# Performance work log

Hardware: AMD Instinct MI355X
Metric: run time of the kernel (lower is better)

## Reference

```python
import jax, jax.numpy as jnp
import numpy as np

NEG_SLOPE = 0.2

def _l2norm(x):
    # F.normalize(x, 2, -1): x / max(||x||_2, 1e-12)
    return x / jnp.maximum(jnp.linalg.norm(x, axis=-1, keepdims=True), 1e-12)

def _segment_softmax(e, dst, n_dst):
    m = jax.ops.segment_max(e, dst, num_segments=n_dst)
    m = jnp.where(jnp.isfinite(m), m, 0.0)
    ex = jnp.exp(e - m[dst])
    denom = jax.ops.segment_sum(ex, dst, num_segments=n_dst)
    return ex / (denom[dst] + 1e-16)

def _gat_conv(x_src, x_dst, edge_index, W, a_src, a_dst, b, n_dst):
    # PyG GATConv, heads=1, concat, shared lin for src/dst (int in_channels)
    h_src = x_src @ W                      # [Ns, H]
    h_dst = x_dst @ W                      # [Nd, H]
    src, dst = edge_index[0], edge_index[1]
    al_s = h_src @ a_src                   # [Ns]
    al_d = h_dst @ a_dst                   # [Nd]
    e = jax.nn.leaky_relu(al_s[src] + al_d[dst], NEG_SLOPE)  # [E]
    coef = _segment_softmax(e, dst, n_dst)                   # [E]
    out = jax.ops.segment_sum(coef[:, None] * h_src[src], dst, num_segments=n_dst)
    return out + b

def setup_inputs() -> dict:
    key = jax.random.key(0)
    ks = jax.random.split(key, 32)
    nd, npr, nc, H, L, B = 2000, 19000, 100, 256, 2, 8192
    E_pp, E_dp, E_cp = 400000, 60000, 300000
    s = 0.1
    inp = {
        'drug_emb': jax.random.normal(ks[0], (nd, H), jnp.float32),
        'protein_emb': jax.random.normal(ks[1], (npr, H), jnp.float32),
        'cell_emb': jax.random.normal(ks[2], (nc, H), jnp.float32),
        'W_pp': jax.random.normal(ks[3], (L, H, H), jnp.float32) * s,
        'as_pp': jax.random.normal(ks[4], (L, H), jnp.float32) * s,
        'ad_pp': jax.random.normal(ks[5], (L, H), jnp.float32) * s,
        'b_pp': jax.random.normal(ks[6], (L, H), jnp.float32) * s,
        'W_dp': jax.random.normal(ks[7], (L, H, H), jnp.float32) * s,
        'as_dp': jax.random.normal(ks[8], (L, H), jnp.float32) * s,
        'ad_dp': jax.random.normal(ks[9], (L, H), jnp.float32) * s,
        'b_dp': jax.random.normal(ks[10], (L, H), jnp.float32) * s,
        'W_cp': jax.random.normal(ks[11], (L, H, H), jnp.float32) * s,
        'as_cp': jax.random.normal(ks[12], (L, H), jnp.float32) * s,
        'ad_cp': jax.random.normal(ks[13], (L, H), jnp.float32) * s,
        'b_cp': jax.random.normal(ks[14], (L, H), jnp.float32) * s,
        'W1': jax.random.normal(ks[15], (3 * H, 6 * H), jnp.float32) * s,
        'b1': jax.random.normal(ks[16], (6 * H,), jnp.float32) * s,
        'W2': jax.random.normal(ks[17], (6 * H, 2 * H), jnp.float32) * s,
        'b2': jax.random.normal(ks[18], (2 * H,), jnp.float32) * s,
        'W3': jax.random.normal(ks[19], (2 * H, 2), jnp.float32) * s,
        'b3': jax.random.normal(ks[20], (2,), jnp.float32) * s,
        'edge_pp': jnp.stack([jax.random.randint(ks[21], (E_pp,), 0, npr),
                              jax.random.randint(ks[22], (E_pp,), 0, npr)]),
        'edge_dp': jnp.stack([jax.random.randint(ks[23], (E_dp,), 0, npr),
                              jax.random.randint(ks[24], (E_dp,), 0, nd)]),
        'edge_cp': jnp.stack([jax.random.randint(ks[25], (E_cp,), 0, npr),
                              jax.random.randint(ks[26], (E_cp,), 0, nc)]),
        'drug1': jax.random.randint(ks[27], (B,), 0, nd),
        'drug2': jax.random.randint(ks[28], (B,), 0, nd),
        'cell': jax.random.randint(ks[29], (B,), 0, nc),
    }
    return inp

def reference(drug_emb, protein_emb, cell_emb,
              W_pp, as_pp, ad_pp, b_pp,
              W_dp, as_dp, ad_dp, b_dp,
              W_cp, as_cp, ad_cp, b_cp,
              W1, b1, W2, b2, W3, b3,
              edge_pp, edge_dp, edge_cp, drug1, drug2, cell):
    n_drug, n_prot, n_cell = drug_emb.shape[0], protein_emb.shape[0], cell_emb.shape[0]
    num_layer = W_pp.shape[0]
    # node ids are arange -> embedding lookup is the full table
    x_d, x_p, x_c = drug_emb, protein_emb, cell_emb
    # p-p GATConv adds self loops (default add_self_loops=True)
    loop = jnp.arange(n_prot, dtype=edge_pp.dtype)
    ei_pp = jnp.concatenate([edge_pp, jnp.stack([loop, loop])], axis=1)
    for l in range(num_layer):
        x_p = _gat_conv(x_p, x_p, ei_pp, W_pp[l], as_pp[l], ad_pp[l], b_pp[l], n_prot)
        x_p = _l2norm(x_p)
        x_d = jax.nn.relu(_gat_conv(x_p, x_d, edge_dp, W_dp[l], as_dp[l], ad_dp[l], b_dp[l], n_drug))
        x_c = jax.nn.relu(_gat_conv(x_p, x_c, edge_cp, W_cp[l], as_cp[l], ad_cp[l], b_cp[l], n_cell))
    hid = jnp.concatenate([_l2norm(x_d[drug1]), _l2norm(x_d[drug2]), _l2norm(x_c[cell])], axis=1)
    h = jax.nn.relu(hid @ W1 + b1)
    h = jax.nn.relu(h @ W2 + b2)
    logits = h @ W3 + b3
    return logits
```

## Files before the change

### kernel.cpp

```cpp
#include <hip/hip_runtime.h>
#include <hip/hip_bf16.h>

#define HDIM 256
#define NEG_SLOPE 0.2f
#define NB 128
#define SLICES 8
#define TBN 64
#define TBK 32

typedef __attribute__((ext_vector_type(8))) short bf16x8;
typedef __attribute__((ext_vector_type(4))) float f32x4;

__device__ inline uint f2pl(float x) {
  __hip_bfloat16 h = __float2bfloat16(x);
  ushort hi = *(ushort*)&h;
  float r = x - __bfloat162float(h);
  __hip_bfloat16 l = __float2bfloat16(r);
  ushort lo = *(ushort*)&l;
  return (uint)hi | ((uint)lo << 16);
}
__device__ inline ushort f2b(float x) {
  __hip_bfloat16 h = __float2bfloat16(x);
  return *(ushort*)&h;
}
__device__ inline float b2f(ushort u) {
  uint x = ((uint)u) << 16;
  return __int_as_float((int)x);
}

static inline int cdiv(int a, int b) { return (a + b - 1) / b; }

__global__ void fillf_kernel(float* __restrict__ p, float v, int n) {
  int i = blockIdx.x * blockDim.x + threadIdx.x;
  if (i < n) p[i] = v;
}

__global__ void fill_out2_kernel(float* __restrict__ out, const float* __restrict__ b3, int M) {
  int i = blockIdx.x * 256 + threadIdx.x;
  if (i >= M) return;
  out[(size_t)i * 2 + 0] = b3[0];
  out[(size_t)i * 2 + 1] = b3[1];
}

__global__ void wconv_split_kernel(const float* __restrict__ W,
                                   ushort* __restrict__ WTh, ushort* __restrict__ WTl,
                                   int K, int N) {
  int i = blockIdx.x * 256 + threadIdx.x;
  if (i >= K * N) return;
  int k = i / N, n = i - k * N;
  uint p = f2pl(W[i]);
  WTh[(size_t)n * K + k] = (ushort)(p & 0xffff);
  WTl[(size_t)n * K + k] = (ushort)(p >> 16);
}

__global__ void wconv_split3_kernel(
    const float* __restrict__ Wpp, const float* __restrict__ Wdp, const float* __restrict__ Wcp,
    ushort* __restrict__ WTpph, ushort* __restrict__ WTppl,
    ushort* __restrict__ WTdph, ushort* __restrict__ WTdpl,
    ushort* __restrict__ WTcph, ushort* __restrict__ WTcpl, int L) {
  const int per = HDIM * HDIM;
  int i = blockIdx.x * 256 + threadIdx.x;
  if (i >= 3 * L * per) return;
  int mat = i / per;
  int r = i - mat * per;
  int l = mat / 3, ty = mat - l * 3;
  const float* W = (ty == 0 ? Wpp : ty == 1 ? Wdp : Wcp) + (size_t)l * per;
  ushort* Th = (ty == 0 ? WTpph : ty == 1 ? WTdph : WTcph) + (size_t)l * per;
  ushort* Tl = (ty == 0 ? WTppl : ty == 1 ? WTdpl : WTcpl) + (size_t)l * per;
  int k = r >> 8, n = r & (HDIM - 1);
  uint p = f2pl(W[r]);
  Th[(size_t)n * HDIM + k] = (ushort)(p & 0xffff);
  Tl[(size_t)n * HDIM + k] = (ushort)(p >> 16);
}

__global__ void f32_to_b16_kernel(const float* __restrict__ in, ushort* __restrict__ out, int n) {
  int i = blockIdx.x * 256 + threadIdx.x;
  if (i < n) out[i] = f2b(in[i]);
}

__global__ void f32_to_split_kernel(const float* __restrict__ in,
                                    ushort* __restrict__ oh, ushort* __restrict__ ol, int n) {
  int i = blockIdx.x * 256 + threadIdx.x;
  if (i >= n) return;
  uint p = f2pl(in[i]);
  oh[i] = (ushort)(p & 0xffff);
  ol[i] = (ushort)(p >> 16);
}

__global__ __launch_bounds__(256) void matvec_all_kernel(
    const float* __restrict__ Wpp, const float* __restrict__ aspp, const float* __restrict__ adpp,
    const float* __restrict__ Wdp, const float* __restrict__ asdp, const float* __restrict__ addp,
    const float* __restrict__ Wcp, const float* __restrict__ ascp, const float* __restrict__ adcp,
    float* __restrict__ wv) {
  int b = blockIdx.x;
  int l = b / 6, r = b - l * 6, type = r >> 1, isd = r & 1;
  const float* W = (type == 0 ? Wpp : type == 1 ? Wdp : Wcp) + (size_t)l * HDIM * HDIM;
  const float* a = (type == 0 ? (isd ? adpp : aspp)
                  : type == 1 ? (isd ? addp : asdp)
                              : (isd ? adcp : ascp)) + (size_t)l * HDIM;
  int k = threadIdx.x;
  const float4* Wr = (const float4*)(W + (size_t)k * HDIM);
  float s = 0.f;
#pragma unroll 8
  for (int n4 = 0; n4 < HDIM / 4; ++n4) {
    float4 w = Wr[n4];
    float4 av = *(const float4*)(a + n4 * 4);
    s += w.x * av.x + w.y * av.y + w.z * av.z + w.w * av.w;
  }
  wv[(size_t)b * HDIM + k] = s;
}

__global__ __launch_bounds__(256) void combine_h1_kernel(
    const float* __restrict__ P1, const float* __restrict__ P2, const float* __restrict__ P3,
    const int* __restrict__ g1, const int* __restrict__ g2, const int* __restrict__ g3,
    int row0, ushort* __restrict__ h1h, ushort* __restrict__ h1l, int M, int K) {
  int t = blockIdx.x * 256 + threadIdx.x;
  int kq = K >> 2;
  if (t >= M * kq) return;
  int row = t / kq, c4 = t - row * kq;
  int bi = row0 + row;
  size_t o = (size_t)c4 * 4;
  float4 a = *(const float4*)(P1 + (size_t)g1[bi] * K + o);
  float4 b = *(const float4*)(P2 + (size_t)g2[bi] * K + o);
  float4 c = *(const float4*)(P3 + (size_t)g3[bi] * K + o);
  uint p0 = f2pl(fmaxf(a.x + b.x + c.x, 0.f));
  uint p1 = f2pl(fmaxf(a.y + b.y + c.y, 0.f));
  uint p2 = f2pl(fmaxf(a.z + b.z + c.z, 0.f));
  uint p3 = f2pl(fmaxf(a.w + b.w + c.w, 0.f));
  ushort4 h = {(ushort)(p0 & 0xffff), (ushort)(p1 & 0xffff), (ushort)(p2 & 0xffff), (ushort)(p3 & 0xffff)};
  ushort4 l = {(ushort)(p0 >> 16), (ushort)(p1 >> 16), (ushort)(p2 >> 16), (ushort)(p3 >> 16)};
  *(ushort4*)(h1h + (size_t)row * K + o) = h;
  *(ushort4*)(h1l + (size_t)row * K + o) = l;
}

template <int TBM_, int ACT, int FUSE3>
__global__ __launch_bounds__(256) void mfma_gemm(
    const ushort* __restrict__ Ahg, const ushort* __restrict__ Alg,
    const ushort* __restrict__ Bhg, const ushort* __restrict__ Blg,
    int ldb, const float* __restrict__ bias, const float* __restrict__ W3g,
    float* __restrict__ C, int M, int N, int K) {
  __shared__ __align__(16) ushort Ah[2][4][TBM_][8];
  __shared__ __align__(16) ushort Al[2][4][TBM_][8];
  __shared__ __align__(16) ushort Bh[2][4][TBN][8];
  __shared__ __align__(16) ushort Bl[2][4][TBN][8];

  constexpr int NU = TBM_ / 64;
  constexpr int TM = TBM_ / 32;

  const int tid = threadIdx.x;
  const int lane = tid & 63;
  const int wid = tid >> 6;
  const int wm = wid & 1, wn = wid >> 1;
  const int l16 = lane & 15;
  const int quad = lane >> 4;
  const int m0 = blockIdx.x * TBM_;
  const int n0 = blockIdx.y * TBN;

  const int gq = lane & 3;
  const int co = gq * 8;
  const int r4 = lane >> 2;

  uint4 rah0[NU], ral0[NU], rbh0, rbl0;
  uint4 rah1[NU], ral1[NU], rbh1, rbl1;

  auto LOADA = [&](uint4* rah, uint4* ral, uint4& rbh, uint4& rbl, int k0) {
#pragma unroll
    for (int u = 0; u < NU; ++u) {
      int r = wid * (TBM_ / 4) + r4 + 16 * u;
      int gm = m0 + r;
      if (gm < M) {
        size_t o = (size_t)gm * K + k0 + co;
        rah[u] = *(const uint4*)(Ahg + o);
        ral[u] = *(const uint4*)(Alg + o);
      } else {
        rah[u] = make_uint4(0, 0, 0, 0);
        ral[u] = make_uint4(0, 0, 0, 0);
      }
    }
    {
      int r = wid * 16 + r4;
      size_t o = (size_t)(n0 + r) * ldb + k0 + co;
      rbh = *(const uint4*)(Bhg + o);
      rbl = *(const uint4*)(Blg + o);
    }
  };
  auto STORE = [&](const uint4* rah, const uint4* ral, const uint4& rbh, const uint4& rbl, int b) {
#pragma unroll
    for (int u = 0; u < NU; ++u) {
      int r = wid * (TBM_ / 4) + r4 + 16 * u;
      *(uint4*)&Ah[b][gq][r][0] = rah[u];
      *(uint4*)&Al[b][gq][r][0] = ral[u];
    }
    int r = wid * 16 + r4;
    *(uint4*)&Bh[b][gq][r][0] = rbh;
    *(uint4*)&Bl[b][gq][r][0] = rbl;
  };

  f32x4 acc[TM][2];
#pragma unroll
  for (int i = 0; i < TM; ++i)
#pragma unroll
    for (int j = 0; j < 2; ++j) acc[i][j] = (f32x4){0.f, 0.f, 0.f, 0.f};

  auto COMPUTE = [&](int b) {
    bf16x8 ahf[TM], alf[TM], bhf[2], blf[2];
#pragma unroll
    for (int t = 0; t < TM; ++t) {
      int r = wm * (TBM_ / 2) + t * 16 + l16;
      ahf[t] = *(const bf16x8*)&Ah[b][quad][r][0];
      alf[t] = *(const bf16x8*)&Al[b][quad][r][0];
    }
#pragma unroll
    for (int t = 0; t < 2; ++t) {
      int r = wn * 32 + t * 16 + l16;
      bhf[t] = *(const bf16x8*)&Bh[b][quad][r][0];
      blf[t] = *(const bf16x8*)&Bl[b][quad][r][0];
    }
#pragma unroll
    for (int tm = 0; tm < TM; ++tm)
#pragma unroll
      for (int tn = 0; tn < 2; ++tn) {
        acc[tm][tn] = __builtin_amdgcn_mfma_f32_16x16x32_bf16(ahf[tm], bhf[tn], acc[tm][tn], 0, 0, 0);
        acc[tm][tn] = __builtin_amdgcn_mfma_f32_16x16x32_bf16(ahf[tm], blf[tn], acc[tm][tn], 0, 0, 0);
        acc[tm][tn] = __builtin_amdgcn_mfma_f32_16x16x32_bf16(alf[tm], bhf[tn], acc[tm][tn], 0, 0, 0);
      }
  };

  const int NK = K / TBK;
  LOADA(rah0, ral0, rbh0, rbl0, 0);
  LOADA(rah1, ral1, rbh1, rbl1, TBK);
  STORE(rah0, ral0, rbh0, rbl0, 0);
  int k = 2 * TBK;
  for (int t = 0; t < (NK - 2) / 2; ++t) {
    __syncthreads();
    LOADA(rah0, ral0, rbh0, rbl0, k);
    COMPUTE(0);
    STORE(rah1, ral1, rbh1, rbl1, 1);
    k += TBK;
    __syncthreads();
    LOADA(rah1, ral1, rbh1, rbl1, k);
    COMPUTE(1);
    STORE(rah0, ral0, rbh0, rbl0, 0);
    k += TBK;
  }
  __syncthreads();
  COMPUTE(0);
  STORE(rah1, ral1, rbh1, rbl1, 1);
  __syncthreads();
  COMPUTE(1);

  if (FUSE3) {
#pragma unroll
    for (int tm = 0; tm < TM; ++tm) {
#pragma unroll
      for (int r = 0; r < 4; ++r) {
        int row = m0 + wm * (TBM_ / 2) + tm * 16 + quad * 4 + r;
        float s0 = 0.f, s1 = 0.f;
#pragma unroll
        for (int tn = 0; tn < 2; ++tn) {
          int col = n0 + wn * 32 + tn * 16 + l16;
          float v = fmaxf(acc[tm][tn][r] + bias[col], 0.f);
          s0 += v * W3g[col * 2 + 0];
          s1 += v * W3g[col * 2 + 1];
        }
#pragma unroll
        for (int o = 1; o < 16; o <<= 1) {
          s0 += __shfl_xor(s0, o);
          s1 += __shfl_xor(s1, o);
        }
        if (l16 == 0 && row < M) {
          atomicAdd(&C[(size_t)row * 2 + 0], s0);
          atomicAdd(&C[(size_t)row * 2 + 1], s1);
        }
      }
    }
  } else {
#pragma unroll
    for (int tn = 0; tn < 2; ++tn) {
      int col = n0 + wn * 32 + tn * 16 + l16;
      float bv = bias ? bias[col] : 0.f;
#pragma unroll
      for (int tm = 0; tm < TM; ++tm) {
#pragma unroll
        for (int r = 0; r < 4; ++r) {
          int row = m0 + wm * (TBM_ / 2) + tm * 16 + quad * 4 + r;
          if (row >= M) continue;
          float v = acc[tm][tn][r] + bv;
          if (ACT == 1) v = fmaxf(v, 0.f);
          C[(size_t)row * N + col] = v;
        }
      }
    }
  }
}

template <int TBM_, int ACT>
static void gemm_launch(hipStream_t s,
                        const ushort* Ahg, const ushort* Alg,
                        const ushort* Bhg, const ushort* Blg,
                        int ldb, const float* bias, float* C,
                        int M, int N, int K) {
  dim3 g(cdiv(M, TBM_), N / TBN);
  mfma_gemm<TBM_, ACT, 0><<<g, 256, 0, s>>>(Ahg, Alg, Bhg, Blg, ldb, bias, nullptr, C, M, N, K);
}

static void gemm_launch_f3(hipStream_t s,
                           const ushort* Ahg, const ushort* Alg,
                           const ushort* Bhg, const ushort* Blg,
                           int ldb, const float* bias, const float* W3,
                           float* C, int M, int N, int K) {
  dim3 g(cdiv(M, 128), N / TBN);
  mfma_gemm<128, 1, 1><<<g, 256, 0, s>>>(Ahg, Alg, Bhg, Blg, ldb, bias, W3, C, M, N, K);
}

__global__ __launch_bounds__(256) void rowdot_kernel(
    const float* __restrict__ H, const float* __restrict__ a,
    float* __restrict__ out, int n) {
  int row = blockIdx.x * 4 + (threadIdx.x >> 6);
  if (row >= n) return;
  int lane = threadIdx.x & 63;
  const float* h = H + (size_t)row * HDIM;
  float s = 0.f;
#pragma unroll
  for (int u = 0; u < 4; ++u) {
    int c = lane + u * 64;
    s += h[c] * a[c];
  }
#pragma unroll
  for (int off = 32; off; off >>= 1) s += __shfl_down(s, off);
  if (lane == 0) out[row] = s;
}

__global__ __launch_bounds__(256) void rowdot2_kernel(
    const float* __restrict__ H, const float* __restrict__ a1, const float* __restrict__ a2,
    float* __restrict__ o1, float* __restrict__ o2, int n) {
  int row = blockIdx.x * 4 + (threadIdx.x >> 6);
  if (row >= n) return;
  int lane = threadIdx.x & 63;
  const float* h = H + (size_t)row * HDIM;
  float s1 = 0.f, s2 = 0.f;
#pragma unroll
  for (int u = 0; u < 4; ++u) {
    int c = lane + u * 64;
    float hv = h[c];
    s1 += hv * a1[c];
    s2 += hv * a2[c];
  }
#pragma unroll
  for (int off = 32; off; off >>= 1) {
    s1 += __shfl_down(s1, off);
    s2 += __shfl_down(s2, off);
  }
  if (lane == 0) { o1[row] = s1; o2[row] = s2; }
}

__global__ __launch_bounds__(256) void hist_kernel(
    const int* __restrict__ src, const int* __restrict__ dst, int E, int nloops,
    int Nd, int* __restrict__ offs) {
  extern __shared__ int bins[];
  int tot = E + nloops;
  int chunk = (tot + NB - 1) / NB;
  int b = blockIdx.x;
  int s0 = b * chunk, s1 = min(s0 + chunk, tot);
  for (int i = threadIdx.x; i < Nd; i += 256) bins[i] = 0;
  __syncthreads();
  for (int i = s0 + threadIdx.x; i < s1; i += 256) {
    int d = (i < E) ? dst[i] : (i - E);
    atomicAdd(&bins[d], 1);
  }
  __syncthreads();
  for (int i = threadIdx.x; i < Nd; i += 256) offs[(size_t)i * NB + b] = bins[i];
}

__global__ __launch_bounds__(256) void scan_bins_kernel(
    int* __restrict__ offs, int* __restrict__ binsum, int Nd) {
  int d = blockIdx.x * 4 + (threadIdx.x >> 6);
  if (d >= Nd) return;
  int lane = threadIdx.x & 63;
  int* p = offs + (size_t)d * NB;
  int v0 = p[2 * lane], v1 = p[2 * lane + 1];
  int s = v0 + v1;
  int t = s;
#pragma unroll
  for (int o = 1; o < 64; o <<= 1) { int u = __shfl_up(t, o); if (lane >= o) t += u; }
  int excl = t - s;
  p[2 * lane] = excl;
  p[2 * lane + 1] = excl + v0;
  if (lane == 63) binsum[d] = t;
}

__global__ __launch_bounds__(256) void scan_base_kernel(
    const int* __restrict__ binsum, int* __restrict__ rowptr, int Nd) {
  __shared__ int wsum[4];
  __shared__ int carry;
  if (threadIdx.x == 0) carry = 0;
  __syncthreads();
  int lane = threadIdx.x & 63, w = threadIdx.x >> 6;
  for (int t0 = 0; t0 < Nd; t0 += 256) {
    int i = t0 + threadIdx.x;
    int v = (i < Nd) ? binsum[i] : 0;
    int t = v;
#pragma unroll
    for (int o = 1; o < 64; o <<= 1) { int u = __shfl_up(t, o); if (lane >= o) t += u; }
    if (lane == 63) wsum[w] = t;
    __syncthreads();
    int add = carry;
    for (int k = 0; k < w; ++k) add += wsum[k];
    if (i < Nd) rowptr[i] = t - v + add;
    __syncthreads();
    if (threadIdx.x == 0) carry += wsum[0] + wsum[1] + wsum[2] + wsum[3];
    __syncthreads();
  }
  if (threadIdx.x == 0) rowptr[Nd] = carry;
}

__global__ __launch_bounds__(256) void scatter_kernel(
    const int* __restrict__ src, const int* __restrict__ dst, int E, int nloops,
    int Nd, const int* __restrict__ offs, const int* __restrict__ rowptr,
    uint* __restrict__ sd) {
  extern __shared__ int bins[];
  int tot = E + nloops;
  int chunk = (tot + NB - 1) / NB;
  int b = blockIdx.x;
  int s0 = b * chunk, s1 = min(s0 + chunk, tot);
  for (int i = threadIdx.x; i < Nd; i += 256) bins[i] = 0;
  __syncthreads();
  for (int i = s0 + threadIdx.x; i < s1; i += 256) {
    int s_, d_;
    if (i < E) { s_ = src[i]; d_ = dst[i]; }
    else       { s_ = d_ = i - E; }
    int local = atomicAdd(&bins[d_], 1);
    int pos = rowptr[d_] + offs[(size_t)d_ * NB + b] + local;
    sd[pos] = (uint)s_ | ((uint)d_ << 16);
  }
}

__global__ __launch_bounds__(256) void gat_agg_split(
    const int* __restrict__ rowptr, const uint* __restrict__ sd,
    const float* __restrict__ als, const float* __restrict__ ald,
    const ushort* __restrict__ Xb,
    ushort* __restrict__ aggh, ushort* __restrict__ aggl, int n) {
  int d = blockIdx.x * 4 + (threadIdx.x >> 6);
  if (d >= n) return;
  int lane = threadIdx.x & 63;
  int r0 = rowptr[d], r1 = rowptr[d + 1];
  float aldd = ald[d];
  float dsum = 0.f;
  for (int j = r0 + lane; j < r1; j += 64) {
    float e = als[sd[j] & 0xffff] + aldd;
    e = (e > 0.f) ? e : NEG_SLOPE * e;
    dsum += __expf(e);
  }
#pragma unroll
  for (int o = 32; o; o >>= 1) dsum += __shfl_xor(dsum, o);
  float rden = 1.f / (dsum + 1e-16f);

  float4 acc = make_float4(0.f, 0.f, 0.f, 0.f);
  for (int b = r0; b < r1; b += 64) {
    int j = b + lane;
    float exv = 0.f; int srcv = 0;
    if (j < r1) {
      uint p = sd[j];
      srcv = p & 0xffff;
      float e = als[srcv] + aldd;
      e = (e > 0.f) ? e : NEG_SLOPE * e;
      exv = __expf(e) * rden;
    }
    int cnt = min(64, r1 - b);
    for (int t0 = 0; t0 < cnt; t0 += 8) {
      float cf[8]; int sv[8];
#pragma unroll
      for (int u = 0; u < 8; ++u) {
        cf[u] = __shfl(exv, t0 + u);
        sv[u] = __shfl(srcv, t0 + u);
      }
      ushort4 hv[8];
#pragma unroll
      for (int u = 0; u < 8; ++u)
        hv[u] = *(const ushort4*)(Xb + (size_t)sv[u] * HDIM + lane * 4);
#pragma unroll
      for (int u = 0; u < 8; ++u) {
        acc.x += cf[u] * b2f(hv[u].x);
        acc.y += cf[u] * b2f(hv[u].y);
        acc.z += cf[u] * b2f(hv[u].z);
        acc.w += cf[u] * b2f(hv[u].w);
      }
    }
  }
  uint p0 = f2pl(acc.x), p1 = f2pl(acc.y), p2 = f2pl(acc.z), p3 = f2pl(acc.w);
  ushort4 h = {(ushort)(p0 & 0xffff), (ushort)(p1 & 0xffff), (ushort)(p2 & 0xffff), (ushort)(p3 & 0xffff)};
  ushort4 l = {(ushort)(p0 >> 16), (ushort)(p1 >> 16), (ushort)(p2 >> 16), (ushort)(p3 >> 16)};
  *(ushort4*)(aggh + (size_t)d * HDIM + lane * 4) = h;
  *(ushort4*)(aggl + (size_t)d * HDIM + lane * 4) = l;
}

__global__ __launch_bounds__(256) void gat_agg_slice(
    const int* __restrict__ rowptr, const uint* __restrict__ sd,
    const float* __restrict__ als, const float* __restrict__ ald,
    const ushort* __restrict__ Xb, float* __restrict__ out32, int n) {
  int d = blockIdx.x / SLICES;
  int sl = blockIdx.x - d * SLICES;
  if (d >= n) return;
  int lane = threadIdx.x & 63, w = threadIdx.x >> 6;
  int r0 = rowptr[d], r1 = rowptr[d + 1];
  float aldd = ald[d];
  float dsum = 0.f;
  for (int j = r0 + threadIdx.x; j < r1; j += 256) {
    float e = als[sd[j] & 0xffff] + aldd;
    e = (e > 0.f) ? e : NEG_SLOPE * e;
    dsum += __expf(e);
  }
#pragma unroll
  for (int o = 32; o; o >>= 1) dsum += __shfl_xor(dsum, o);
  __shared__ float wd[4];
  if (lane == 0) wd[w] = dsum;
  __syncthreads();
  float rden = 1.f / (wd[0] + wd[1] + wd[2] + wd[3] + 1e-16f);
  int deg = r1 - r0;
  int per_b = (deg + SLICES - 1) / SLICES;
  int b0 = r0 + sl * per_b, b1 = min(b0 + per_b, r1);
  int wdeg = b1 - b0;
  if (wdeg <= 0) return;
  int per_w = (wdeg + 3) >> 2;
  int w0 = b0 + w * per_w, w1 = min(w0 + per_w, b1);

  float4 acc = make_float4(0.f, 0.f, 0.f, 0.f);
  for (int b = w0; b < w1; b += 64) {
    int j = b + lane;
    float exv = 0.f; int srcv = 0;
    if (j < w1) {
      uint p = sd[j];
      srcv = p & 0xffff;
      float e = als[srcv] + aldd;
      e = (e > 0.f) ? e : NEG_SLOPE * e;
      exv = __expf(e) * rden;
    }
    int cnt = min(64, w1 - b);
    for (int t0 = 0; t0 < cnt; t0 += 8) {
      float cf[8]; int sv[8];
#pragma unroll
      for (int u = 0; u < 8; ++u) {
        cf[u] = __shfl(exv, t0 + u);
        sv[u] = __shfl(srcv, t0 + u);
      }
      ushort4 hv[8];
#pragma unroll
      for (int u = 0; u < 8; ++u)
        hv[u] = *(const ushort4*)(Xb + (size_t)sv[u] * HDIM + lane * 4);
#pragma unroll
      for (int u = 0; u < 8; ++u) {
        acc.x += cf[u] * b2f(hv[u].x);
        acc.y += cf[u] * b2f(hv[u].y);
        acc.z += cf[u] * b2f(hv[u].z);
        acc.w += cf[u] * b2f(hv[u].w);
      }
    }
  }
  float* o = out32 + (size_t)d * HDIM + lane * 4;
  atomicAdd(o + 0, acc.x); atomicAdd(o + 1, acc.y);
  atomicAdd(o + 2, acc.z); atomicAdd(o + 3, acc.w);
}

__global__ __launch_bounds__(256) void l2norm_f32b_dots_kernel(
    const float* __restrict__ in, float* __restrict__ outf, ushort* __restrict__ outb,
    const float* __restrict__ v1, const float* __restrict__ v2,
    const float* __restrict__ v3, const float* __restrict__ v4,
    float* __restrict__ o1, float* __restrict__ o2,
    float* __restrict__ o3, float* __restrict__ o4, int n) {
  int row = blockIdx.x * 4 + (threadIdx.x >> 6);
  if (row >= n) return;
  int lane = threadIdx.x & 63;
  float v[4];
  float ss = 0.f;
#pragma unroll
  for (int u = 0; u < 4; ++u) {
    float t = in[(size_t)row * HDIM + lane + u * 64];
    v[u] = t; ss += t * t;
  }
#pragma unroll
  for (int off = 32; off; off >>= 1) ss += __shfl_xor(ss, off);
  float sc = 1.0f / fmaxf(sqrtf(ss), 1e-12f);
  float d1 = 0.f, d2 = 0.f, d3 = 0.f, d4 = 0.f;
#pragma unroll
  for (int u = 0; u < 4; ++u) {
    float f = v[u] * sc;
    int c = lane + u * 64;
    outf[(size_t)row * HDIM + c] = f;
    outb[(size_t)row * HDIM + c] = f2b(f);
    d1 += f * v1[c];
    d2 += f * v2[c];
    if (o3) { d3 += f * v3[c]; d4 += f * v4[c]; }
  }
#pragma unroll
  for (int off = 32; off; off >>= 1) {
    d1 += __shfl_xor(d1, off);
    d2 += __shfl_xor(d2, off);
    if (o3) { d3 += __shfl_xor(d3, off); d4 += __shfl_xor(d4, off); }
  }
  if (lane == 0) {
    o1[row] = d1; o2[row] = d2;
    if (o3) { o3[row] = d3; o4[row] = d4; }
  }
}

__global__ __launch_bounds__(256) void l2norm_split_kernel(
    const float* __restrict__ in,
    ushort* __restrict__ oh, ushort* __restrict__ ol, int n) {
  int row = blockIdx.x * 4 + (threadIdx.x >> 6);
  if (row >= n) return;
  int lane = threadIdx.x & 63;
  float v[4];
  float ss = 0.f;
#pragma unroll
  for (int u = 0; u < 4; ++u) {
    int c = lane + u * 64;
    float t = in[(size_t)row * HDIM + c];
    v[u] = t;
    ss += t * t;
  }
#pragma unroll
  for (int off = 32; off; off >>= 1) ss += __shfl_xor(ss, off);
  float sc = 1.0f / fmaxf(sqrtf(ss), 1e-12f);
#pragma unroll
  for (int u = 0; u < 4; ++u) {
    int c = lane + u * 64;
    uint p = f2pl(v[u] * sc);
    oh[(size_t)row * HDIM + c] = (ushort)(p & 0xffff);
    ol[(size_t)row * HDIM + c] = (ushort)(p >> 16);
  }
}

static void build_sorted(hipStream_t stream,
                         const int* src, const int* dst, int E, int nloops, int Nd,
                         int* offs, int* binsum, int* rowptr, uint* sd) {
  size_t lds = (size_t)Nd * sizeof(int);
  hist_kernel<<<NB, 256, lds, stream>>>(src, dst, E, nloops, Nd, offs);
  scan_bins_kernel<<<cdiv(Nd, 4), 256, 0, stream>>>(offs, binsum, Nd);
  scan_base_kernel<<<1, 256, 0, stream>>>(binsum, rowptr, Nd);
  scatter_kernel<<<NB, 256, lds, stream>>>(src, dst, E, nloops, Nd, offs, rowptr, sd);
}

extern "C" void kernel_launch(void* const* d_in, const int* in_sizes, int n_in,
                              void* d_out, int out_size, void* d_ws, size_t ws_size,
                              hipStream_t stream) {
  const float* drug_emb = (const float*)d_in[0];
  const float* prot_emb = (const float*)d_in[1];
  const float* cell_emb = (const float*)d_in[2];
  const float* W_pp = (const float*)d_in[3];
  const float* as_pp = (const float*)d_in[4];
  const float* ad_pp = (const float*)d_in[5];
  const float* b_pp = (const float*)d_in[6];
  const float* W_dp = (const float*)d_in[7];
  const float* as_dp = (const float*)d_in[8];
  const float* ad_dp = (const float*)d_in[9];
  const float* b_dp = (const float*)d_in[10];
  const float* W_cp = (const float*)d_in[11];
  const float* as_cp = (const float*)d_in[12];
  const float* ad_cp = (const float*)d_in[13];
  const float* b_cp = (const float*)d_in[14];
  const float* W1 = (const float*)d_in[15];
  const float* b1 = (const float*)d_in[16];
  const float* W2 = (const float*)d_in[17];
  const float* b2 = (const float*)d_in[18];
  const float* W3 = (const float*)d_in[19];
  const float* b3 = (const float*)d_in[20];
  const int* edge_pp = (const int*)d_in[21];
  const int* edge_dp = (const int*)d_in[22];
  const int* edge_cp = (const int*)d_in[23];
  const int* drug1 = (const int*)d_in[24];
  const int* drug2 = (const int*)d_in[25];
  const int* cellb = (const int*)d_in[26];

  const int ND = in_sizes[0] / HDIM;
  const int NP = in_sizes[1] / HDIM;
  const int NC = in_sizes[2] / HDIM;
  const int L = in_sizes[3] / (HDIM * HDIM);
  const int E_pp = in_sizes[21] / 2;
  const int E_dp = in_sizes[22] / 2;
  const int E_cp = in_sizes[23] / 2;
  const int B = in_sizes[24];
  (void)n_in; (void)out_size;

  const int* src_pp = edge_pp;          const int* dst_pp = edge_pp + E_pp;
  const int* src_dp = edge_dp;          const int* dst_dp = edge_dp + E_dp;
  const int* src_cp = edge_cp;          const int* dst_cp = edge_cp + E_cp;
  const int tot_pp = E_pp + NP, tot_dp = E_dp, tot_cp = E_cp;
  int maxN = NP > ND ? NP : ND; if (NC > maxN) maxN = NC;

  char* wsb = (char*)d_ws;
  size_t off = 0;
  auto alloc = [&](size_t bytes) -> void* {
    void* p = wsb + off;
    off += (bytes + 255) & ~(size_t)255;
    return p;
  };

  float* Xp  = (float*)alloc((size_t)NP * HDIM * 4);
  ushort* Xpb = (ushort*)alloc((size_t)NP * HDIM * 2);
  float* Xd  = (float*)alloc((size_t)ND * HDIM * 4);
  float* Xc  = (float*)alloc((size_t)NC * HDIM * 4);
  ushort* xdnh = (ushort*)alloc((size_t)ND * HDIM * 2);
  ushort* xdnl = (ushort*)alloc((size_t)ND * HDIM * 2);
  ushort* xcnh = (ushort*)alloc((size_t)NC * HDIM * 2);
  ushort* xcnl = (ushort*)alloc((size_t)NC * HDIM * 2);
  ushort* WTpph = (ushort*)alloc((size_t)L * HDIM * HDIM * 2);
  ushort* WTppl = (ushort*)alloc((size_t)L * HDIM * HDIM * 2);
  ushort* WTdph = (ushort*)alloc((size_t)L * HDIM * HDIM * 2);
  ushort* WTdpl = (ushort*)alloc((size_t)L * HDIM * HDIM * 2);
  ushort* WTcph = (ushort*)alloc((size_t)L * HDIM * HDIM * 2);
  ushort* WTcpl = (ushort*)alloc((size_t)L * HDIM * HDIM * 2);
  ushort* cth = (ushort*)alloc((size_t)NC * HDIM * 2);
  ushort* ctl = (ushort*)alloc((size_t)NC * HDIM * 2);
  float* wv  = (float*)alloc((size_t)L * 6 * HDIM * 4);
  float* pals = (float*)alloc((size_t)maxN * 4);
  float* pald = (float*)alloc((size_t)maxN * 4);
  float* als1 = (float*)alloc((size_t)maxN * 4);
  float* als2 = (float*)alloc((size_t)maxN * 4);
  float* ald1 = (float*)alloc((size_t)maxN * 4);
  float* ald2 = (float*)alloc((size_t)maxN * 4);
  int* binsum = (int*)alloc((size_t)maxN * 4);
  int* rp_pp = (int*)alloc((size_t)(NP + 1) * 4);
  int* rp_dp = (int*)alloc((size_t)(ND + 1) * 4);
  int* rp_cp = (int*)alloc((size_t)(NC + 1) * 4);
  uint* sd_pp = (uint*)alloc((size_t)tot_pp * 4);
  uint* sd_dp = (uint*)alloc((size_t)tot_dp * 4);
  uint* sd_cp = (uint*)alloc((size_t)tot_cp * 4);
  float* out32 = (float*)alloc((size_t)NC * HDIM * 4);
  size_t S0 = off;

  int* offs = (int*)(wsb + S0);
  build_sorted(stream, src_pp, dst_pp, E_pp, NP, NP, offs, binsum, rp_pp, sd_pp);
  build_sorted(stream, src_dp, dst_dp, E_dp, 0, ND, offs, binsum, rp_dp, sd_dp);
  build_sorted(stream, src_cp, dst_cp, E_cp, 0, NC, offs, binsum, rp_cp, sd_cp);

  wconv_split3_kernel<<<cdiv(3 * L * HDIM * HDIM, 256), 256, 0, stream>>>(
      W_pp, W_dp, W_cp, WTpph, WTppl, WTdph, WTdpl, WTcph, WTcpl, L);
  matvec_all_kernel<<<L * 6, 256, 0, stream>>>(W_pp, as_pp, ad_pp, W_dp, as_dp, ad_dp,
                                               W_cp, as_cp, ad_cp, wv);
  f32_to_b16_kernel<<<cdiv(NP * HDIM, 256), 256, 0, stream>>>(prot_emb, Xpb, NP * HDIM);

  size_t aggB = ((size_t)NP * HDIM * 2 + 255) & ~(size_t)255;
  ushort* aggh = (ushort*)(wsb + S0);
  ushort* aggl = (ushort*)(wsb + S0 + aggB);
  float* tmp = (float*)(wsb + S0 + 2 * aggB);

  rowdot2_kernel<<<cdiv(NP, 4), 256, 0, stream>>>(prot_emb, wv + 0 * HDIM, wv + 1 * HDIM,
                                                  pals, pald, NP);

  for (int l = 0; l < L; ++l) {
    const int WOFF = l * HDIM * HDIM, VOFF = l * HDIM;
    const float* wvl = wv + (size_t)l * 6 * HDIM;
    const float* wvn = wv + (size_t)(l + 1) * 6 * HDIM;
    const float* Xd_cur = (l == 0) ? drug_emb : Xd;
    const float* Xc_cur = (l == 0) ? cell_emb : Xc;
    bool last = (l == L - 1);

    gat_agg_split<<<cdiv(NP, 4), 256, 0, stream>>>(rp_pp, sd_pp, pals, pald, Xpb, aggh, aggl, NP);
    gemm_launch<128, 0>(stream, aggh, aggl, WTpph + WOFF, WTppl + WOFF, HDIM,
                        b_pp + VOFF, tmp, NP, HDIM, HDIM);
    l2norm_f32b_dots_kernel<<<cdiv(NP, 4), 256, 0, stream>>>(
        tmp, Xp, Xpb,
        wvl + 2 * HDIM, wvl + 4 * HDIM,
        last ? nullptr : (wvn + 0 * HDIM), last ? nullptr : (wvn + 1 * HDIM),
        als1, als2, last ? nullptr : pals, last ? nullptr : pald, NP);

    rowdot_kernel<<<cdiv(ND, 4), 256, 0, stream>>>(Xd_cur, wvl + 3 * HDIM, ald1, ND);
    rowdot_kernel<<<cdiv(NC, 4), 256, 0, stream>>>(Xc_cur, wvl + 5 * HDIM, ald2, NC);

    gat_agg_split<<<cdiv(ND, 4), 256, 0, stream>>>(rp_dp, sd_dp, als1, ald1, Xpb, aggh, aggl, ND);
    gemm_launch<64, 1>(stream, aggh, aggl, WTdph + WOFF, WTdpl + WOFF, HDIM,
                       b_dp + VOFF, Xd, ND, HDIM, HDIM);

    fillf_kernel<<<cdiv(NC * HDIM, 256), 256, 0, stream>>>(out32, 0.f, NC * HDIM);
    gat_agg_slice<<<NC * SLICES, 256, 0, stream>>>(rp_cp, sd_cp, als2, ald2, Xpb, out32, NC);
    f32_to_split_kernel<<<cdiv(NC * HDIM, 256), 256, 0, stream>>>(out32, cth, ctl, NC * HDIM);
    gemm_launch<64, 1>(stream, cth, ctl, WTcph + WOFF, WTcpl + WOFF, HDIM,
                       b_cp + VOFF, Xc, NC, HDIM, HDIM);
  }

  l2norm_split_kernel<<<cdiv(ND, 4), 256, 0, stream>>>(Xd, xdnh, xdnl, ND);
  l2norm_split_kernel<<<cdiv(NC, 4), 256, 0, stream>>>(Xc, xcnh, xcnl, NC);

  const int N1 = 6 * HDIM;
  const int N2 = 2 * HDIM;
  const int K1 = 3 * HDIM;
  ushort* W1Th = (ushort*)(wsb + S0);
  ushort* W1Tl = W1Th + (size_t)N1 * K1;
  ushort* W2Th = W1Tl + (size_t)N1 * K1;
  ushort* W2Tl = W2Th + (size_t)N2 * N1;
  float* P1 = (float*)(W2Tl + (size_t)N2 * N1);
  float* P2 = P1 + (size_t)ND * N1;
  float* P3 = P2 + (size_t)ND * N1;
  ushort* h1h = (ushort*)(P3 + (size_t)NC * N1);
  size_t wsz = ws_size ? ws_size : ((size_t)1 << 30);
  size_t fixed = S0 + ((size_t)N1 * K1 + (size_t)N2 * N1) * 4
               + ((size_t)(2 * ND + NC) * N1) * 4;
  int CH = 8192;
  while (CH > 1024 && fixed + (size_t)CH * N1 * 4 > wsz) CH >>= 1;
  ushort* h1l = h1h + (size_t)CH * N1;

  wconv_split_kernel<<<cdiv(K1 * N1, 256), 256, 0, stream>>>(W1, W1Th, W1Tl, K1, N1);
  wconv_split_kernel<<<cdiv(N1 * N2, 256), 256, 0, stream>>>(W2, W2Th, W2Tl, N1, N2);

  gemm_launch<64, 0>(stream, xdnh, xdnl, W1Th, W1Tl, K1, nullptr, P1, ND, N1, HDIM);
  gemm_launch<64, 0>(stream, xdnh, xdnl, W1Th + HDIM, W1Tl + HDIM, K1, nullptr, P2, ND, N1, HDIM);
  gemm_launch<64, 0>(stream, xcnh, xcnl, W1Th + 2 * HDIM, W1Tl + 2 * HDIM, K1, b1, P3, NC, N1, HDIM);

  float* outp = (float*)d_out;
  fill_out2_kernel<<<cdiv(B, 256), 256, 0, stream>>>(outp, b3, B);
  for (int c0 = 0; c0 < B; c0 += CH) {
    int M = (B - c0) < CH ? (B - c0) : CH;
    combine_h1_kernel<<<cdiv(M * (N1 / 4), 256), 256, 0, stream>>>(
        P1, P2, P3, drug1, drug2, cellb, c0, h1h, h1l, M, N1);
    gemm_launch_f3(stream, h1h, h1l, W2Th, W2Tl, N1, b2, W3,
                   outp + (size_t)c0 * 2, M, N2, N1);
  }
}
```

Before: 714.9 us.

## Swizzle GEMM LDS layout to avoid bank conflicts and fuse protein prep kernels

Reorganizes the MFMA GEMM shared-memory tiles into 16-row chunks with an XOR-like slot rotation based on the k-quad, so that stores and fragment loads spread across LDS banks instead of conflicting. It also fuses the f32-to-bf16 conversion of the protein embedding with the two attention row-dot products into one kernel, which saves a full extra read of the protein table and one launch. The swizzle adds index arithmetic and must stay consistent between store and load paths. The wvn pointer change only avoids forming an out-of-range pointer on the last layer.

```diff
diff --git a/kernel.cpp b/kernel.cpp
--- a/kernel.cpp
+++ b/kernel.cpp
@@ -108,6 +108,30 @@
     s += w.x * av.x + w.y * av.y + w.z * av.z + w.w * av.w;
   }
   wv[(size_t)b * HDIM + k] = s;
+}
+
+__global__ __launch_bounds__(256) void prep_p_kernel(
+    const float* __restrict__ in, ushort* __restrict__ outb,
+    const float* __restrict__ a1, const float* __restrict__ a2,
+    float* __restrict__ o1, float* __restrict__ o2, int n) {
+  int row = blockIdx.x * 4 + (threadIdx.x >> 6);
+  if (row >= n) return;
+  int lane = threadIdx.x & 63;
+  float s1 = 0.f, s2 = 0.f;
+#pragma unroll
+  for (int u = 0; u < 4; ++u) {
+    int c = lane + u * 64;
+    float hv = in[(size_t)row * HDIM + c];
+    outb[(size_t)row * HDIM + c] = f2b(hv);
+    s1 += hv * a1[c];
+    s2 += hv * a2[c];
+  }
+#pragma unroll
+  for (int off = 32; off; off >>= 1) {
+    s1 += __shfl_down(s1, off);
+    s2 += __shfl_down(s2, off);
+  }
+  if (lane == 0) { o1[row] = s1; o2[row] = s2; }
 }
 
 __global__ __launch_bounds__(256) void combine_h1_kernel(
@@ -139,10 +163,10 @@
     const ushort* __restrict__ Bhg, const ushort* __restrict__ Blg,
     int ldb, const float* __restrict__ bias, const float* __restrict__ W3g,
     float* __restrict__ C, int M, int N, int K) {
-  __shared__ __align__(16) ushort Ah[2][4][TBM_][8];
-  __shared__ __align__(16) ushort Al[2][4][TBM_][8];
-  __shared__ __align__(16) ushort Bh[2][4][TBN][8];
-  __shared__ __align__(16) ushort Bl[2][4][TBN][8];
+  __shared__ __align__(16) ushort Ah[2][4][TBM_ / 16][16][8];
+  __shared__ __align__(16) ushort Al[2][4][TBM_ / 16][16][8];
+  __shared__ __align__(16) ushort Bh[2][4][TBN / 16][16][8];
+  __shared__ __align__(16) ushort Bl[2][4][TBN / 16][16][8];
 
   constexpr int NU = TBM_ / 64;
   constexpr int TM = TBM_ / 32;
@@ -159,6 +183,8 @@
   const int gq = lane & 3;
   const int co = gq * 8;
   const int r4 = lane >> 2;
+  const int wslot = (r4 + 2 * gq) & 15;
+  const int rslot = (l16 + 2 * quad) & 15;
 
   uint4 rah0[NU], ral0[NU], rbh0, rbl0;
   uint4 rah1[NU], ral1[NU], rbh1, rbl1;
@@ -187,13 +213,12 @@
   auto STORE = [&](const uint4* rah, const uint4* ral, const uint4& rbh, const uint4& rbl, int b) {
 #pragma unroll
     for (int u = 0; u < NU; ++u) {
-      int r = wid * (TBM_ / 4) + r4 + 16 * u;
-      *(uint4*)&Ah[b][gq][r][0] = rah[u];
-      *(uint4*)&Al[b][gq][r][0] = ral[u];
-    }
-    int r = wid * 16 + r4;
-    *(uint4*)&Bh[b][gq][r][0] = rbh;
-    *(uint4*)&Bl[b][gq][r][0] = rbl;
+      int ch = (wid * (TBM_ / 4) + 16 * u) >> 4;
+      *(uint4*)&Ah[b][gq][ch][wslot][0] = rah[u];
+      *(uint4*)&Al[b][gq][ch][wslot][0] = ral[u];
+    }
+    *(uint4*)&Bh[b][gq][wid][wslot][0] = rbh;
+    *(uint4*)&Bl[b][gq][wid][wslot][0] = rbl;
   };
 
   f32x4 acc[TM][2];
@@ -206,15 +231,15 @@
     bf16x8 ahf[TM], alf[TM], bhf[2], blf[2];
 #pragma unroll
     for (int t = 0; t < TM; ++t) {
-      int r = wm * (TBM_ / 2) + t * 16 + l16;
-      ahf[t] = *(const bf16x8*)&Ah[b][quad][r][0];
-      alf[t] = *(const bf16x8*)&Al[b][quad][r][0];
+      int ch = wm * (TBM_ / 32) + t;
+      ahf[t] = *(const bf16x8*)&Ah[b][quad][ch][rslot][0];
+      alf[t] = *(const bf16x8*)&Al[b][quad][ch][rslot][0];
     }
 #pragma unroll
     for (int t = 0; t < 2; ++t) {
-      int r = wn * 32 + t * 16 + l16;
-      bhf[t] = *(const bf16x8*)&Bh[b][quad][r][0];
-      blf[t] = *(const bf16x8*)&Bl[b][quad][r][0];
+      int ch = wn * 2 + t;
+      bhf[t] = *(const bf16x8*)&Bh[b][quad][ch][rslot][0];
+      blf[t] = *(const bf16x8*)&Bl[b][quad][ch][rslot][0];
     }
 #pragma unroll
     for (int tm = 0; tm < TM; ++tm)
@@ -737,23 +762,21 @@
       W_pp, W_dp, W_cp, WTpph, WTppl, WTdph, WTdpl, WTcph, WTcpl, L);
   matvec_all_kernel<<<L * 6, 256, 0, stream>>>(W_pp, as_pp, ad_pp, W_dp, as_dp, ad_dp,
                                                W_cp, as_cp, ad_cp, wv);
-  f32_to_b16_kernel<<<cdiv(NP * HDIM, 256), 256, 0, stream>>>(prot_emb, Xpb, NP * HDIM);
+  prep_p_kernel<<<cdiv(NP, 4), 256, 0, stream>>>(prot_emb, Xpb, wv + 0 * HDIM, wv + 1 * HDIM,
+                                                 pals, pald, NP);
 
   size_t aggB = ((size_t)NP * HDIM * 2 + 255) & ~(size_t)255;
   ushort* aggh = (ushort*)(wsb + S0);
   ushort* aggl = (ushort*)(wsb + S0 + aggB);
   float* tmp = (float*)(wsb + S0 + 2 * aggB);
 
-  rowdot2_kernel<<<cdiv(NP, 4), 256, 0, stream>>>(prot_emb, wv + 0 * HDIM, wv + 1 * HDIM,
-                                                  pals, pald, NP);
-
   for (int l = 0; l < L; ++l) {
     const int WOFF = l * HDIM * HDIM, VOFF = l * HDIM;
     const float* wvl = wv + (size_t)l * 6 * HDIM;
-    const float* wvn = wv + (size_t)(l + 1) * 6 * HDIM;
+    bool last = (l == L - 1);
+    const float* wvn = last ? wvl : wv + (size_t)(l + 1) * 6 * HDIM;
     const float* Xd_cur = (l == 0) ? drug_emb : Xd;
     const float* Xc_cur = (l == 0) ? cell_emb : Xc;
-    bool last = (l == L - 1);
 
     gat_agg_split<<<cdiv(NP, 4), 256, 0, stream>>>(rp_pp, sd_pp, pals, pald, Xpb, aggh, aggl, NP);
     gemm_launch<128, 0>(stream, aggh, aggl, WTpph + WOFF, WTppl + WOFF, HDIM,
```

New measurement: 697.8 us. 2.4% less time.
